# Performance work log

Hardware: AMD Instinct MI355X
Metric: run time of the kernel (lower is better)

## Reference

```python
import jax, jax.numpy as jnp
import numpy as np

HIDDEN = 1024
NUM_HEADS = 16
HEAD_DIM = HIDDEN // NUM_HEADS
WINDOW = 64
B, S = 2, 4096


def setup_inputs() -> dict:
    key = jax.random.key(0)
    ks = jax.random.split(key, 8)
    d = {
        'query': jax.random.normal(ks[0], (B, S, HIDDEN), jnp.float32),
        'key':   jax.random.normal(ks[1], (B, S, HIDDEN), jnp.float32),
        'value': jax.random.normal(ks[2], (B, S, HIDDEN), jnp.float32),
        'Wq': jax.random.normal(ks[3], (HIDDEN, HIDDEN), jnp.float32) * 0.02,
        'bq': jnp.zeros((HIDDEN,), jnp.float32),
        'Wk': jax.random.normal(ks[4], (HIDDEN, HIDDEN), jnp.float32) * 0.02,
        'bk': jnp.zeros((HIDDEN,), jnp.float32),
        'Wv': jax.random.normal(ks[5], (HIDDEN, HIDDEN), jnp.float32) * 0.02,
        'bv': jnp.zeros((HIDDEN,), jnp.float32),
        'Wo': jax.random.normal(ks[6], (HIDDEN, HIDDEN), jnp.float32) * 0.02,
        'bo': jnp.zeros((HIDDEN,), jnp.float32),
    }
    return d


def reference(query, key, value, Wq, bq, Wk, bk, Wv, bv, Wo, bo):
    b, s, _ = query.shape
    h, d, w = NUM_HEADS, HEAD_DIM, WINDOW
    nw = s // w
    scale = d ** -0.5
    # projections (torch Linear: x @ W.T + b)
    q = (query @ Wq.T + bq).reshape(b, s, h, d).transpose(0, 2, 1, 3)  # [b,h,s,d]
    k = (key   @ Wk.T + bk).reshape(b, s, h, d).transpose(0, 2, 1, 3)
    v = (value @ Wv.T + bv).reshape(b, s, h, d).transpose(0, 2, 1, 3)
    # split into non-overlapping windows: [b,h,nw,w,d]
    qw = q.reshape(b, h, nw, w, d)
    kw = k.reshape(b, h, nw, w, d)
    vw = v.reshape(b, h, nw, w, d)
    scores = jnp.einsum('bhnqd,bhnkd->bhnqk', qw, kw) * scale  # [b,h,nw,w,w]
    weights = jax.nn.softmax(scores, axis=-1)
    attended = jnp.einsum('bhnqk,bhnkd->bhnqd', weights, vw)   # [b,h,nw,w,d]
    attended = attended.reshape(b, h, s, d).transpose(0, 2, 1, 3).reshape(b, s, h * d)
    output = attended @ Wo.T + bo
    # block-diagonal attention map, averaged over heads -> [b,s,s]
    mean_w = weights.mean(axis=1)  # [b,nw,w,w]
    full = jnp.zeros((b, nw, w, nw, w), weights.dtype)
    idx = jnp.arange(nw)
    full = full.at[:, idx, :, idx, :].set(mean_w.transpose(1, 0, 2, 3))
    attn = full.reshape(b, s, s)
    return output, attn
```

## Files before the change

kernel.cpp:

```cpp
#include <hip/hip_runtime.h>

typedef unsigned short u16;
typedef unsigned int u32;
typedef __attribute__((ext_vector_type(8))) short bf16x8;
typedef __attribute__((ext_vector_type(4))) float f32x4;
typedef __attribute__((ext_vector_type(4))) u16 u16x4;

typedef __attribute__((address_space(1))) unsigned int as1_u32;
typedef __attribute__((address_space(3))) unsigned int as3_u32;

#define SEQ 4096
#define HID 1024
#define NHEAD 16
#define BATCH 2

__device__ __forceinline__ u16 f2b(float f) {
  union { float f; u32 u; } v; v.f = f;
  u32 r = v.u + 0x7FFFu + ((v.u >> 16) & 1u);
  return (u16)(r >> 16);
}

__device__ __forceinline__ float b2f(u16 b) {
  union { u32 u; float f; } v; v.u = ((u32)b) << 16;
  return v.f;
}

__device__ __forceinline__ void async_cp16(const void* g, void* l) {
  __builtin_amdgcn_global_load_lds((const as1_u32*)g, (as3_u32*)l, 16, 0, 0);
}

__global__ __launch_bounds__(256) void cvt_all(
    const float* __restrict__ q, const float* __restrict__ k, const float* __restrict__ v,
    const float* __restrict__ Wq, const float* __restrict__ Wk,
    const float* __restrict__ Wv, const float* __restrict__ Wo,
    u16* __restrict__ xq, u16* __restrict__ xk, u16* __restrict__ xv,
    u16* __restrict__ wq, u16* __restrict__ wk, u16* __restrict__ wv, u16* __restrict__ wo) {
  const int total = (3 << 21) + (4 << 18);
  for (int i = blockIdx.x * blockDim.x + threadIdx.x; i < total; i += gridDim.x * blockDim.x) {
    const float* src; u16* dst; int j;
    if (i < (3 << 21)) {
      const int sel = i >> 21; j = i & ((1 << 21) - 1);
      src = sel == 0 ? q : (sel == 1 ? k : v);
      dst = sel == 0 ? xq : (sel == 1 ? xk : xv);
    } else {
      const int ii = i - (3 << 21);
      const int sel = ii >> 18; j = ii & ((1 << 18) - 1);
      src = sel == 0 ? Wq : (sel == 1 ? Wk : (sel == 2 ? Wv : Wo));
      dst = sel == 0 ? wq : (sel == 1 ? wk : (sel == 2 ? wv : wo));
    }
    float4 f = ((const float4*)src)[j];
    u16x4 o; o.x = f2b(f.x); o.y = f2b(f.y); o.z = f2b(f.z); o.w = f2b(f.w);
    ((u16x4*)dst)[j] = o;
  }
}

struct Gemm3Args {
  const u16* A[3]; const u16* W[3]; const float* bias[3]; void* C[3]; int mode[3];
};

__global__ __launch_bounds__(256, 2) void gemm_bt_fused(Gemm3Args ga) {
  __shared__ __align__(16) u16 As[128 * 32];
  __shared__ __align__(16) u16 Bs[128 * 32];

  const int z = blockIdx.z;
  const u16* __restrict__ A  = ga.A[z];
  const u16* __restrict__ Bw = ga.W[z];
  const float* __restrict__ bias = ga.bias[z];
  void* __restrict__ Cout = ga.C[z];
  const int mode = ga.mode[z];
  const int K = HID, N = HID;

  const int tid = threadIdx.x;
  const int lane = tid & 63;
  const int wave = tid >> 6;
  const int l15 = lane & 15;
  const int quad = lane >> 4;
  const int wr = wave >> 1;
  const int wc = wave & 1;
  const long brow = (long)blockIdx.y * 128;
  const long bcol = (long)blockIdx.x * 128;

  const int srow = lane >> 2;
  const int scol = (lane & 3) * 8;
  const u16* Ag0 = A + (brow + wave * 16 + srow) * (long)K + scol;
  const u16* Ag1 = A + (brow + (wave + 4) * 16 + srow) * (long)K + scol;
  const u16* Bg0 = Bw + (bcol + wave * 16 + srow) * (long)K + scol;
  const u16* Bg1 = Bw + (bcol + (wave + 4) * 16 + srow) * (long)K + scol;
  u16* Al0 = As + wave * 512;
  u16* Al1 = As + (wave + 4) * 512;
  u16* Bl0 = Bs + wave * 512;
  u16* Bl1 = Bs + (wave + 4) * 512;

  f32x4 acc[4][4];
#pragma unroll
  for (int i = 0; i < 4; ++i)
#pragma unroll
    for (int j = 0; j < 4; ++j) acc[i][j] = f32x4{0.f, 0.f, 0.f, 0.f};

  const u16* Afb = As + (wr * 64 + l15) * 32 + quad * 8;
  const u16* Bfb = Bs + (wc * 64 + l15) * 32 + quad * 8;

  for (int k0 = 0; k0 < K; k0 += 32) {
    async_cp16(Ag0 + k0, Al0);
    async_cp16(Ag1 + k0, Al1);
    async_cp16(Bg0 + k0, Bl0);
    async_cp16(Bg1 + k0, Bl1);
    __syncthreads();
    bf16x8 af[4], bfv[4];
#pragma unroll
    for (int mt = 0; mt < 4; ++mt) af[mt] = *(const bf16x8*)(Afb + mt * 512);
#pragma unroll
    for (int nt = 0; nt < 4; ++nt) bfv[nt] = *(const bf16x8*)(Bfb + nt * 512);
#pragma unroll
    for (int mt = 0; mt < 4; ++mt)
#pragma unroll
      for (int nt = 0; nt < 4; ++nt)
        acc[mt][nt] = __builtin_amdgcn_mfma_f32_16x16x32_bf16(af[mt], bfv[nt], acc[mt][nt], 0, 0, 0);
    __syncthreads();
  }

  const long crow0 = brow + wr * 64;
  const long ccol0 = bcol + wc * 64;
#pragma unroll
  for (int nt = 0; nt < 4; ++nt) {
    const long col = ccol0 + nt * 16 + l15;
    const float bv = bias[col];
    if (mode == 2) {
#pragma unroll
      for (int mt = 0; mt < 4; ++mt) {
        const long tokbase = crow0 + mt * 16 + quad * 4;
        const long b = tokbase >> 12;
        const long tok = tokbase & 4095;
        const long h = col >> 6, d = col & 63;
        u16x4 pk;
        pk.x = f2b(acc[mt][nt][0] + bv);
        pk.y = f2b(acc[mt][nt][1] + bv);
        pk.z = f2b(acc[mt][nt][2] + bv);
        pk.w = f2b(acc[mt][nt][3] + bv);
        *(u16x4*)((u16*)Cout + ((b * 16 + h) * 64 + d) * (long)SEQ + tok) = pk;
      }
    } else if (mode == 1) {
#pragma unroll
      for (int mt = 0; mt < 4; ++mt)
#pragma unroll
        for (int r = 0; r < 4; ++r) {
          const long row = crow0 + mt * 16 + quad * 4 + r;
          ((float*)Cout)[row * (long)N + col] = acc[mt][nt][r] + bv;
        }
    } else {
#pragma unroll
      for (int mt = 0; mt < 4; ++mt)
#pragma unroll
        for (int r = 0; r < 4; ++r) {
          const long row = crow0 + mt * 16 + quad * 4 + r;
          ((u16*)Cout)[row * (long)N + col] = f2b(acc[mt][nt][r] + bv);
        }
    }
  }
}

__global__ __launch_bounds__(256, 4) void attn_win(
    const u16* __restrict__ qp, const u16* __restrict__ kp,
    const u16* __restrict__ vT, u16* __restrict__ attended,
    float* __restrict__ attn) {
  __shared__ __align__(16) u16 Plds[4][32][72];

  const int tid = threadIdx.x;
  const int lane = tid & 63;
  const int wave = tid >> 6;
  const int l15 = lane & 15;
  const int quad = lane >> 4;

  const int idx = blockIdx.x;
  const int half = idx & 1;
  const int hg = (idx >> 1) & 3;
  const int wn = idx >> 3;
  const int b = wn >> 6;
  const int n = wn & 63;
  const int h = hg * 4 + wave;

  const long qrow0 = (long)b * SEQ + (long)n * 64 + half * 32;
  const long krow0 = (long)b * SEQ + (long)n * 64;
  const long cbase = (long)h * 64;

  u16(*Pw)[72] = Plds[wave];

  f32x4 s[2][4];
#pragma unroll
  for (int i = 0; i < 2; ++i)
#pragma unroll
    for (int j = 0; j < 4; ++j) s[i][j] = f32x4{0.f, 0.f, 0.f, 0.f};
#pragma unroll
  for (int kt = 0; kt < 2; ++kt) {
    bf16x8 aq[2], bkf[4];
#pragma unroll
    for (int mt = 0; mt < 2; ++mt)
      aq[mt] = *(const bf16x8*)(qp + (qrow0 + mt * 16 + l15) * HID + cbase + kt * 32 + quad * 8);
#pragma unroll
    for (int nt = 0; nt < 4; ++nt)
      bkf[nt] = *(const bf16x8*)(kp + (krow0 + nt * 16 + l15) * HID + cbase + kt * 32 + quad * 8);
#pragma unroll
    for (int mt = 0; mt < 2; ++mt)
#pragma unroll
      for (int nt = 0; nt < 4; ++nt)
        s[mt][nt] = __builtin_amdgcn_mfma_f32_16x16x32_bf16(aq[mt], bkf[nt], s[mt][nt], 0, 0, 0);
  }

#pragma unroll
  for (int mt = 0; mt < 2; ++mt) {
#pragma unroll
    for (int r = 0; r < 4; ++r) {
      float m = -1e30f;
#pragma unroll
      for (int nt = 0; nt < 4; ++nt) { s[mt][nt][r] *= 0.125f; m = fmaxf(m, s[mt][nt][r]); }
      m = fmaxf(m, __shfl_xor(m, 1));
      m = fmaxf(m, __shfl_xor(m, 2));
      m = fmaxf(m, __shfl_xor(m, 4));
      m = fmaxf(m, __shfl_xor(m, 8));
      float sum = 0.f;
#pragma unroll
      for (int nt = 0; nt < 4; ++nt) { float e = __expf(s[mt][nt][r] - m); s[mt][nt][r] = e; sum += e; }
      sum += __shfl_xor(sum, 1);
      sum += __shfl_xor(sum, 2);
      sum += __shfl_xor(sum, 4);
      sum += __shfl_xor(sum, 8);
      const float inv = 1.f / sum;
#pragma unroll
      for (int nt = 0; nt < 4; ++nt) s[mt][nt][r] *= inv;
    }
  }

#pragma unroll
  for (int mt = 0; mt < 2; ++mt)
#pragma unroll
    for (int nt = 0; nt < 4; ++nt)
#pragma unroll
      for (int r = 0; r < 4; ++r)
        Pw[mt * 16 + quad * 4 + r][nt * 16 + l15] = f2b(s[mt][nt][r]);

  f32x4 o[2][4];
#pragma unroll
  for (int i = 0; i < 2; ++i)
#pragma unroll
    for (int j = 0; j < 4; ++j) o[i][j] = f32x4{0.f, 0.f, 0.f, 0.f};
  const long vbase = ((long)(b * 16 + h) * 64) * SEQ;
#pragma unroll
  for (int kt = 0; kt < 2; ++kt) {
    bf16x8 ap[2], bvf[4];
#pragma unroll
    for (int mt = 0; mt < 2; ++mt)
      ap[mt] = *(const bf16x8*)(&Pw[mt * 16 + l15][kt * 32 + quad * 8]);
#pragma unroll
    for (int nt = 0; nt < 4; ++nt)
      bvf[nt] = *(const bf16x8*)(vT + vbase + (long)(nt * 16 + l15) * SEQ + n * 64 + kt * 32 + quad * 8);
#pragma unroll
    for (int mt = 0; mt < 2; ++mt)
#pragma unroll
      for (int nt = 0; nt < 4; ++nt)
        o[mt][nt] = __builtin_amdgcn_mfma_f32_16x16x32_bf16(ap[mt], bvf[nt], o[mt][nt], 0, 0, 0);
  }

#pragma unroll
  for (int mt = 0; mt < 2; ++mt)
#pragma unroll
    for (int nt = 0; nt < 4; ++nt)
#pragma unroll
      for (int r = 0; r < 4; ++r)
        attended[(qrow0 + mt * 16 + quad * 4 + r) * HID + cbase + nt * 16 + l15] = f2b(o[mt][nt][r]);

  __syncthreads();
  float* obase = attn + (long)b * SEQ * SEQ + ((long)n * 64 + half * 32) * SEQ + (long)n * 64;
  for (int i = tid; i < 32 * 64; i += 256) {
    const int r = i >> 6, c = i & 63;
    float sacc = 0.f;
#pragma unroll
    for (int w = 0; w < 4; ++w) sacc += b2f(Plds[w][r][c]);
    atomicAdd(&obase[(long)r * SEQ + c], sacc * (1.f / 16.f));
  }
}

extern "C" void kernel_launch(void* const* d_in, const int* in_sizes, int n_in,
                              void* d_out, int out_size, void* d_ws, size_t ws_size,
                              hipStream_t stream) {
  (void)in_sizes; (void)n_in; (void)out_size; (void)ws_size;
  const float* query = (const float*)d_in[0];
  const float* key   = (const float*)d_in[1];
  const float* value = (const float*)d_in[2];
  const float* Wq = (const float*)d_in[3];
  const float* bq = (const float*)d_in[4];
  const float* Wk = (const float*)d_in[5];
  const float* bk = (const float*)d_in[6];
  const float* Wv = (const float*)d_in[7];
  const float* bv = (const float*)d_in[8];
  const float* Wo = (const float*)d_in[9];
  const float* bo = (const float*)d_in[10];

  float* out  = (float*)d_out;
  float* attn = out + (size_t)BATCH * SEQ * HID;

  char* ws = (char*)d_ws;
  const size_t MB = (size_t)1 << 20;
  u16* xq = (u16*)(ws + 0 * MB);
  u16* xk = (u16*)(ws + 16 * MB);
  u16* xv = (u16*)(ws + 32 * MB);
  u16* wq = (u16*)(ws + 48 * MB);
  u16* wk = (u16*)(ws + 50 * MB);
  u16* wv = (u16*)(ws + 52 * MB);
  u16* wo = (u16*)(ws + 54 * MB);
  u16* qp = (u16*)(ws + 56 * MB);
  u16* kp = (u16*)(ws + 72 * MB);
  u16* vT  = xk;
  u16* att = xq;

  hipMemsetAsync(attn, 0, (size_t)BATCH * SEQ * SEQ * sizeof(float), stream);

  cvt_all<<<3584, 256, 0, stream>>>(query, key, value, Wq, Wk, Wv, Wo,
                                    xq, xk, xv, wq, wk, wv, wo);

  Gemm3Args ga;
  ga.A[0] = xq; ga.W[0] = wq; ga.bias[0] = bq; ga.C[0] = qp; ga.mode[0] = 0;
  ga.A[1] = xk; ga.W[1] = wk; ga.bias[1] = bk; ga.C[1] = kp; ga.mode[1] = 0;
  ga.A[2] = xv; ga.W[2] = wv; ga.bias[2] = bv; ga.C[2] = vT; ga.mode[2] = 2;
  dim3 g3(HID / 128, (BATCH * SEQ) / 128, 3);
  gemm_bt_fused<<<g3, 256, 0, stream>>>(ga);

  attn_win<<<BATCH * 64 * 4 * 2, 256, 0, stream>>>(qp, kp, vT, att, attn);

  Gemm3Args go;
  go.A[0] = att; go.W[0] = wo; go.bias[0] = bo; go.C[0] = out; go.mode[0] = 1;
  go.A[1] = att; go.W[1] = wo; go.bias[1] = bo; go.C[1] = out; go.mode[1] = 1;
  go.A[2] = att; go.W[2] = wo; go.bias[2] = bo; go.C[2] = out; go.mode[2] = 1;
  dim3 g1(HID / 128, (BATCH * SEQ) / 128, 1);
  gemm_bt_fused<<<g1, 256, 0, stream>>>(go);
}
```

Before: 416.7 us.

## Fuse attention-map expansion into output GEMM launch, drop memset and atomics

The 128 MB memset of the attention map and the atomicAdd scatter of head-averaged weights are removed. Each attention block now writes its per-window partial sums to a compact workspace buffer. A new combined kernel runs the output projection GEMM in its first 512 blocks. Its remaining blocks write the whole dense attention map in a single streaming pass: zeros off the diagonal, the reduced head mean on the diagonal. This avoids writing the map twice plus atomic read-modify-writes, and lets the bandwidth-bound fill overlap with the GEMM. It needs extra workspace for the partial sums and a separate V-transpose buffer.

Result: faster. 407.0 us (-2.3%).

```diff
diff --git a/kernel.cpp b/kernel.cpp
--- a/kernel.cpp
+++ b/kernel.cpp
@@ -139,14 +139,6 @@
         pk.w = f2b(acc[mt][nt][3] + bv);
         *(u16x4*)((u16*)Cout + ((b * 16 + h) * 64 + d) * (long)SEQ + tok) = pk;
       }
-    } else if (mode == 1) {
-#pragma unroll
-      for (int mt = 0; mt < 4; ++mt)
-#pragma unroll
-        for (int r = 0; r < 4; ++r) {
-          const long row = crow0 + mt * 16 + quad * 4 + r;
-          ((float*)Cout)[row * (long)N + col] = acc[mt][nt][r] + bv;
-        }
     } else {
 #pragma unroll
       for (int mt = 0; mt < 4; ++mt)
@@ -162,7 +154,7 @@
 __global__ __launch_bounds__(256, 4) void attn_win(
     const u16* __restrict__ qp, const u16* __restrict__ kp,
     const u16* __restrict__ vT, u16* __restrict__ attended,
-    float* __restrict__ attn) {
+    float* __restrict__ Psum) {
   __shared__ __align__(16) u16 Plds[4][32][72];
 
   const int tid = threadIdx.x;
@@ -269,13 +261,118 @@
         attended[(qrow0 + mt * 16 + quad * 4 + r) * HID + cbase + nt * 16 + l15] = f2b(o[mt][nt][r]);
 
   __syncthreads();
-  float* obase = attn + (long)b * SEQ * SEQ + ((long)n * 64 + half * 32) * SEQ + (long)n * 64;
+  float* pbase = Psum + (long)idx * 2048;
   for (int i = tid; i < 32 * 64; i += 256) {
     const int r = i >> 6, c = i & 63;
     float sacc = 0.f;
 #pragma unroll
     for (int w = 0; w < 4; ++w) sacc += b2f(Plds[w][r][c]);
-    atomicAdd(&obase[(long)r * SEQ + c], sacc * (1.f / 16.f));
+    pbase[i] = sacc;
+  }
+}
+
+__global__ __launch_bounds__(256, 2) void gemm_o_expand(
+    const u16* __restrict__ A, const u16* __restrict__ Bw,
+    const float* __restrict__ bias, float* __restrict__ Cout,
+    const float* __restrict__ Psum, float* __restrict__ attn) {
+  __shared__ __align__(16) u16 As[128 * 32];
+  __shared__ __align__(16) u16 Bs[128 * 32];
+
+  const int tid = threadIdx.x;
+
+  if (blockIdx.x >= 512) {
+    const long e = blockIdx.x - 512;
+    const long f0 = e * 4096;
+#pragma unroll
+    for (int it = 0; it < 16; ++it) {
+      const long f = f0 + it * 256 + tid;
+      const int b = (int)(f >> 22);
+      const int rem = (int)(f & ((1 << 22) - 1));
+      const int row = rem >> 10;
+      const int c4 = rem & 1023;
+      const int n = row >> 6;
+      float4 val = {0.f, 0.f, 0.f, 0.f};
+      const int d4 = c4 - n * 16;
+      if ((unsigned)d4 < 16u) {
+        const int r = row & 63;
+        const int half = r >> 5, rr = r & 31;
+        const long base = ((long)((b * 64 + n) * 8 + half)) * 2048 + rr * 64 + d4 * 4;
+        float4 p0 = *(const float4*)(Psum + base);
+        float4 p1 = *(const float4*)(Psum + base + 4096);
+        float4 p2 = *(const float4*)(Psum + base + 8192);
+        float4 p3 = *(const float4*)(Psum + base + 12288);
+        val.x = (p0.x + p1.x + p2.x + p3.x) * (1.f / 16.f);
+        val.y = (p0.y + p1.y + p2.y + p3.y) * (1.f / 16.f);
+        val.z = (p0.z + p1.z + p2.z + p3.z) * (1.f / 16.f);
+        val.w = (p0.w + p1.w + p2.w + p3.w) * (1.f / 16.f);
+      }
+      ((float4*)attn)[f] = val;
+    }
+    return;
+  }
+
+  const int lane = tid & 63;
+  const int wave = tid >> 6;
+  const int l15 = lane & 15;
+  const int quad = lane >> 4;
+  const int wr = wave >> 1;
+  const int wc = wave & 1;
+  const long brow = (long)(blockIdx.x >> 3) * 128;
+  const long bcol = (long)(blockIdx.x & 7) * 128;
+  const int K = HID, N = HID;
+
+  const int srow = lane >> 2;
+  const int scol = (lane & 3) * 8;
+  const u16* Ag0 = A + (brow + wave * 16 + srow) * (long)K + scol;
+  const u16* Ag1 = A + (brow + (wave + 4) * 16 + srow) * (long)K + scol;
+  const u16* Bg0 = Bw + (bcol + wave * 16 + srow) * (long)K + scol;
+  const u16* Bg1 = Bw + (bcol + (wave + 4) * 16 + srow) * (long)K + scol;
+  u16* Al0 = As + wave * 512;
+  u16* Al1 = As + (wave + 4) * 512;
+  u16* Bl0 = Bs + wave * 512;
+  u16* Bl1 = Bs + (wave + 4) * 512;
+
+  f32x4 acc[4][4];
+#pragma unroll
+  for (int i = 0; i < 4; ++i)
+#pragma unroll
+    for (int j = 0; j < 4; ++j) acc[i][j] = f32x4{0.f, 0.f, 0.f, 0.f};
+
+  const u16* Afb = As + (wr * 64 + l15) * 32 + quad * 8;
+  const u16* Bfb = Bs + (wc * 64 + l15) * 32 + quad * 8;
+
+  for (int k0 = 0; k0 < K; k0 += 32) {
+    async_cp16(Ag0 + k0, Al0);
+    async_cp16(Ag1 + k0, Al1);
+    async_cp16(Bg0 + k0, Bl0);
+    async_cp16(Bg1 + k0, Bl1);
+    __syncthreads();
+    bf16x8 af[4], bfv[4];
+#pragma unroll
+    for (int mt = 0; mt < 4; ++mt) af[mt] = *(const bf16x8*)(Afb + mt * 512);
+#pragma unroll
+    for (int nt = 0; nt < 4; ++nt) bfv[nt] = *(const bf16x8*)(Bfb + nt * 512);
+#pragma unroll
+    for (int mt = 0; mt < 4; ++mt)
+#pragma unroll
+      for (int nt = 0; nt < 4; ++nt)
+        acc[mt][nt] = __builtin_amdgcn_mfma_f32_16x16x32_bf16(af[mt], bfv[nt], acc[mt][nt], 0, 0, 0);
+    __syncthreads();
+  }
+
+  const long crow0 = brow + wr * 64;
+  const long ccol0 = bcol + wc * 64;
+#pragma unroll
+  for (int nt = 0; nt < 4; ++nt) {
+    const long col = ccol0 + nt * 16 + l15;
+    const float bv = bias[col];
+#pragma unroll
+    for (int mt = 0; mt < 4; ++mt)
+#pragma unroll
+      for (int r = 0; r < 4; ++r) {
+        const long row = crow0 + mt * 16 + quad * 4 + r;
+        Cout[row * (long)N + col] = acc[mt][nt][r] + bv;
+      }
   }
 }
 
@@ -309,10 +406,9 @@
   u16* wo = (u16*)(ws + 54 * MB);
   u16* qp = (u16*)(ws + 56 * MB);
   u16* kp = (u16*)(ws + 72 * MB);
-  u16* vT  = xk;
+  u16* vT = (u16*)(ws + 88 * MB);
+  float* Psum = (float*)(ws + 104 * MB);
   u16* att = xq;
-
-  hipMemsetAsync(attn, 0, (size_t)BATCH * SEQ * SEQ * sizeof(float), stream);
 
   cvt_all<<<3584, 256, 0, stream>>>(query, key, value, Wq, Wk, Wv, Wo,
                                     xq, xk, xv, wq, wk, wv, wo);
@@ -324,12 +420,7 @@
   dim3 g3(HID / 128, (BATCH * SEQ) / 128, 3);
   gemm_bt_fused<<<g3, 256, 0, stream>>>(ga);
 
-  attn_win<<<BATCH * 64 * 4 * 2, 256, 0, stream>>>(qp, kp, vT, att, attn);
-
-  Gemm3Args go;
-  go.A[0] = att; go.W[0] = wo; go.bias[0] = bo; go.C[0] = out; go.mode[0] = 1;
-  go.A[1] = att; go.W[1] = wo; go.bias[1] = bo; go.C[1] = out; go.mode[1] = 1;
-  go.A[2] = att; go.W[2] = wo; go.bias[2] = bo; go.C[2] = out; go.mode[2] = 1;
-  dim3 g1(HID / 128, (BATCH * SEQ) / 128, 1);
-  gemm_bt_fused<<<g1, 256, 0, stream>>>(go);
-}
+  attn_win<<<BATCH * 64 * 4 * 2, 256, 0, stream>>>(qp, kp, vT, att, Psum);
+
+  gemm_o_expand<<<512 + 2048, 256, 0, stream>>>(att, wo, bo, out, Psum, attn);
+}
```
